# Optimization experiments

Measured on AMD Instinct MI355X. Metric: run time of the kernel, lower is better.

The kernel has to match this reference:

```python
import jax, jax.numpy as jnp
import numpy as np

N = 50000
IN_C = 512
HID = 16
HEADS = 3
OUT_C = 128
NEG_SLOPE = 0.2


def _add_self_loops(edge_index, n):
    loop = jnp.arange(n, dtype=edge_index.dtype)
    src = jnp.concatenate([edge_index[0], loop])
    dst = jnp.concatenate([edge_index[1], loop])
    return src, dst


def gat_conv(x, W, a_src, a_dst, b, src, dst, n):
    # x: [N, Fin], W: [Fin, H*C], a_src/a_dst: [H, C], b: [H*C]
    H, C = a_src.shape
    h = (x @ W).reshape(n, H, C)                      # [N, H, C]
    e_src = jnp.einsum('nhc,hc->nh', h, a_src)        # [N, H]
    e_dst = jnp.einsum('nhc,hc->nh', h, a_dst)        # [N, H]
    e = jax.nn.leaky_relu(e_src[src] + e_dst[dst], NEG_SLOPE)  # [E, H]
    # segment softmax over incoming edges of each destination node
    m = jax.ops.segment_max(e, dst, num_segments=n)
    e = jnp.exp(e - m[dst])
    s = jax.ops.segment_sum(e, dst, num_segments=n)
    alpha = e / s[dst]                                 # [E, H]
    out = jax.ops.segment_sum(h[src] * alpha[:, :, None], dst, num_segments=n)
    return out.reshape(n, H * C) + b


def gcn_conv(x, W, b, src, dst, n):
    h = x @ W                                          # [N, Fout]
    ones = jnp.ones(src.shape[0], dtype=h.dtype)
    deg = jax.ops.segment_sum(ones, dst, num_segments=n)
    dinv = jax.lax.rsqrt(jnp.maximum(deg, 1.0))
    norm = dinv[src] * dinv[dst]                       # [E]
    out = jax.ops.segment_sum(h[src] * norm[:, None], dst, num_segments=n)
    return out + b


def setup_inputs() -> dict:
    key = jax.random.key(0)
    ks = jax.random.split(key, 16)
    E = 800000
    x = jax.random.normal(ks[0], (N, IN_C), dtype=jnp.float32)
    edge_index = jax.random.randint(ks[1], (2, E), 0, N, dtype=jnp.int64)

    def glorot(k, shape):
        fan = shape[0] + shape[-1]
        return jax.random.uniform(k, shape, jnp.float32, -1.0, 1.0) * np.sqrt(6.0 / fan)

    return {
        'x': x,
        'edge_index': edge_index,
        'W1': glorot(ks[2], (IN_C, HEADS * HID)),
        'a_src1': glorot(ks[3], (HEADS, HID)),
        'a_dst1': glorot(ks[4], (HEADS, HID)),
        'b1': jnp.zeros((HEADS * HID,), jnp.float32),
        'W2': glorot(ks[5], (HEADS * HID, OUT_C)),
        'a_src2': glorot(ks[6], (1, OUT_C)),
        'a_dst2': glorot(ks[7], (1, OUT_C)),
        'b2': jnp.zeros((OUT_C,), jnp.float32),
        'Wg': glorot(ks[8], (OUT_C, OUT_C)),
        'bg': jnp.zeros((OUT_C,), jnp.float32),
        'Wl': glorot(ks[9], (OUT_C, OUT_C)),
        'bl': jnp.zeros((OUT_C,), jnp.float32),
    }


def reference(x, edge_index, W1, a_src1, a_dst1, b1, W2, a_src2, a_dst2, b2, Wg, bg, Wl, bl):
    n = x.shape[0]
    src, dst = _add_self_loops(edge_index, n)
    # GATModel: gat1 (3 heads, concat) -> elu -> gat2 (1 head) -> log_softmax
    h = gat_conv(x, W1, a_src1, a_dst1, b1, src, dst, n)
    h = jax.nn.elu(h)
    h = gat_conv(h, W2, a_src2, a_dst2, b2, src, dst, n)
    h = jax.nn.log_softmax(h, axis=1)
    # GCN: only conv1 is used in its forward, followed by relu
    h = jax.nn.relu(gcn_conv(h, Wg, bg, src, dst, n))
    # Linear1
    return h @ Wl + bl
```

## Files before the change

### kernel.cpp

```cpp
#include <hip/hip_runtime.h>
#include <hip/hip_bf16.h>
#include <math.h>

#define NN 50000
#define EE 800000
#define ET 850000
#define NB 196
#define NEG 0.2f

static __device__ __forceinline__ float lrelu(float x){ return x > 0.f ? x : NEG * x; }
static __device__ __forceinline__ void edge_sd(const int* __restrict__ ei, int e, int& s, int& d){
  if (e < EE){ s = ei[e]; d = ei[e + EE]; } else { s = e - EE; d = s; }
}

__global__ __launch_bounds__(256) void k_hist(const int* __restrict__ ei, int* __restrict__ deg_i)
{
  int e = blockIdx.x * 256 + threadIdx.x;
  if (e >= ET) return;
  int s, d; edge_sd(ei, e, s, d);
  atomicAdd(deg_i + d, 1);
}

__global__ __launch_bounds__(256) void k_scan_part(const int* __restrict__ deg_i, int* __restrict__ bsum)
{
  __shared__ int wsum[4];
  int t = threadIdx.x;
  int i = blockIdx.x * 256 + t;
  int v = (i < NN) ? deg_i[i] : 0;
  int r = v;
#pragma unroll
  for (int off = 32; off; off >>= 1) r += __shfl_xor(r, off);
  if ((t & 63) == 0) wsum[t >> 6] = r;
  __syncthreads();
  if (t == 0) bsum[blockIdx.x] = wsum[0] + wsum[1] + wsum[2] + wsum[3];
}

__global__ __launch_bounds__(256) void k_scan_top(const int* __restrict__ bsum, int* __restrict__ boff)
{
  __shared__ int bs[256];
  int t = threadIdx.x;
  int v = (t < NB) ? bsum[t] : 0;
  bs[t] = v;
  __syncthreads();
  for (int off = 1; off < 256; off <<= 1){
    int add = (t >= off) ? bs[t - off] : 0;
    __syncthreads();
    bs[t] += add;
    __syncthreads();
  }
  if (t < NB) boff[t] = bs[t] - v;
}

__global__ __launch_bounds__(256) void k_scan_fin(const int* __restrict__ deg_i,
    const int* __restrict__ boff, int* __restrict__ row_start, float* __restrict__ dinv)
{
  __shared__ int bs[256];
  int t = threadIdx.x;
  int i = blockIdx.x * 256 + t;
  int v = (i < NN) ? deg_i[i] : 0;
  bs[t] = v;
  __syncthreads();
  for (int off = 1; off < 256; off <<= 1){
    int add = (t >= off) ? bs[t - off] : 0;
    __syncthreads();
    bs[t] += add;
    __syncthreads();
  }
  if (i < NN){
    row_start[i] = boff[blockIdx.x] + bs[t] - v;
    dinv[i] = rsqrtf(fmaxf((float)v, 1.0f));
  }
  if (i == 0) row_start[NN] = ET;
}

__global__ __launch_bounds__(256) void k_fill(const int* __restrict__ ei,
    const int* __restrict__ row_start, int* __restrict__ cur, int* __restrict__ csr)
{
  int e = blockIdx.x * 256 + threadIdx.x;
  if (e >= ET) return;
  int s, d; edge_sd(ei, e, s, d);
  int pos = atomicAdd(cur + d, 1);
  csr[row_start[d] + pos] = s;
}

__global__ __launch_bounds__(256) void k_gat1_gemm(
    const float* __restrict__ x, const float* __restrict__ W1,
    const float* __restrict__ as1, const float* __restrict__ ad1,
    float* __restrict__ h1, float* __restrict__ es1, float* __restrict__ ed1)
{
  __shared__ float At[64][69];
  __shared__ float Bs[64][52];
  int t = threadIdx.x;
  int tx = t & 15, ty = t >> 4;
  int n0 = blockIdx.x * 64;
  float acc[4][3] = {};
  for (int kt = 0; kt < 512; kt += 64){
    __syncthreads();
#pragma unroll
    for (int p = 0; p < 4; ++p){
      int f = t + p * 256;
      int node = f >> 4, kq = f & 15;
      float4 v = make_float4(0.f, 0.f, 0.f, 0.f);
      int gn = n0 + node;
      if (gn < NN) v = *(const float4*)(x + (size_t)gn * 512 + kt + kq * 4);
      At[kq * 4 + 0][node] = v.x; At[kq * 4 + 1][node] = v.y;
      At[kq * 4 + 2][node] = v.z; At[kq * 4 + 3][node] = v.w;
    }
#pragma unroll
    for (int p = 0; p < 3; ++p){
      int f = t + p * 256;
      int k = f / 12, oq = f % 12;
      *(float4*)&Bs[k][oq * 4] = *(const float4*)(W1 + (size_t)(kt + k) * 48 + oq * 4);
    }
    __syncthreads();
#pragma unroll 8
    for (int k = 0; k < 64; ++k){
      float4 a = *(const float4*)&At[k][ty * 4];
      float b0 = Bs[k][tx * 3 + 0], b1 = Bs[k][tx * 3 + 1], b2 = Bs[k][tx * 3 + 2];
      float av[4] = {a.x, a.y, a.z, a.w};
#pragma unroll
      for (int i = 0; i < 4; ++i){
        acc[i][0] = fmaf(av[i], b0, acc[i][0]);
        acc[i][1] = fmaf(av[i], b1, acc[i][1]);
        acc[i][2] = fmaf(av[i], b2, acc[i][2]);
      }
    }
  }
#pragma unroll
  for (int i = 0; i < 4; ++i){
    int gn = n0 + ty * 4 + i;
    float ps0 = 0.f, ps1 = 0.f, ps2 = 0.f, pd0 = 0.f, pd1 = 0.f, pd2 = 0.f;
#pragma unroll
    for (int j = 0; j < 3; ++j){
      int o = tx * 3 + j;
      int h = o >> 4;
      float a = acc[i][j];
      float vs = a * as1[o], vd = a * ad1[o];
      if (h == 0){ ps0 += vs; pd0 += vd; }
      else if (h == 1){ ps1 += vs; pd1 += vd; }
      else { ps2 += vs; pd2 += vd; }
    }
#pragma unroll
    for (int off = 1; off < 16; off <<= 1){
      ps0 += __shfl_xor(ps0, off, 16); ps1 += __shfl_xor(ps1, off, 16); ps2 += __shfl_xor(ps2, off, 16);
      pd0 += __shfl_xor(pd0, off, 16); pd1 += __shfl_xor(pd1, off, 16); pd2 += __shfl_xor(pd2, off, 16);
    }
    if (gn < NN){
      float* o = h1 + (size_t)gn * 48 + tx * 3;
      o[0] = acc[i][0]; o[1] = acc[i][1]; o[2] = acc[i][2];
      if (tx == 0){
        es1[(size_t)gn * 3 + 0] = ps0; es1[(size_t)gn * 3 + 1] = ps1; es1[(size_t)gn * 3 + 2] = ps2;
        ed1[(size_t)gn * 3 + 0] = pd0; ed1[(size_t)gn * 3 + 1] = pd1; ed1[(size_t)gn * 3 + 2] = pd2;
      }
    }
  }
}

__global__ __launch_bounds__(256) void k_gat1_agg(
    const int* __restrict__ csr, const int* __restrict__ row_start,
    const float* __restrict__ es1, const float* __restrict__ ed1,
    const float* __restrict__ h1, const float* __restrict__ b1,
    float* __restrict__ o1)
{
  int dn = (blockIdx.x * 256 + threadIdx.x) >> 6;
  int lane = threadIdx.x & 63;
  if (dn >= NN) return;
  bool act = lane < 48;
  int hd = act ? (lane >> 4) : 0;
  int beg = row_start[dn], end = row_start[dn + 1];
  float edv = ed1[(size_t)dn * 3 + hd];
  float m = -INFINITY, sum = 0.f, acc = 0.f;
  int i = beg;
  for (; i + 1 < end; i += 2){
    int s0 = csr[i], s1 = csr[i + 1];
    float e0 = lrelu(es1[(size_t)s0 * 3 + hd] + edv);
    float e1 = lrelu(es1[(size_t)s1 * 3 + hd] + edv);
    float h0 = act ? h1[(size_t)s0 * 48 + lane] : 0.f;
    float h1v = act ? h1[(size_t)s1 * 48 + lane] : 0.f;
    float mn = fmaxf(m, fmaxf(e0, e1));
    float sc = __expf(m - mn), w0 = __expf(e0 - mn), w1 = __expf(e1 - mn);
    sum = sum * sc + w0 + w1;
    acc = acc * sc + h0 * w0 + h1v * w1;
    m = mn;
  }
  if (i < end){
    int s0 = csr[i];
    float e0 = lrelu(es1[(size_t)s0 * 3 + hd] + edv);
    float h0 = act ? h1[(size_t)s0 * 48 + lane] : 0.f;
    float mn = fmaxf(m, e0);
    float sc = __expf(m - mn), w0 = __expf(e0 - mn);
    sum = sum * sc + w0;
    acc = acc * sc + h0 * w0;
  }
  if (act){
    float v = acc / sum + b1[lane];
    o1[(size_t)dn * 48 + lane] = v > 0.f ? v : expm1f(v);
  }
}

__global__ __launch_bounds__(256) void k_gat2_gemm(const float* __restrict__ o1,
    const float* __restrict__ W2, const float* __restrict__ as2, const float* __restrict__ ad2,
    float* __restrict__ h2, float* __restrict__ es2, float* __restrict__ ed2)
{
  __shared__ float At[48][68];
  __shared__ float Ws[48][128];
  int t = threadIdx.x, tx = t & 15, ty = t >> 4;
  int n0 = blockIdx.x * 64;
#pragma unroll
  for (int p = 0; p < 3; ++p){
    int f = t + p * 256;
    int node = f / 12, kq = f % 12;
    float4 v = make_float4(0.f, 0.f, 0.f, 0.f);
    if (n0 + node < NN) v = *(const float4*)(o1 + (size_t)(n0 + node) * 48 + kq * 4);
    At[kq * 4 + 0][node] = v.x; At[kq * 4 + 1][node] = v.y;
    At[kq * 4 + 2][node] = v.z; At[kq * 4 + 3][node] = v.w;
  }
#pragma unroll
  for (int p = 0; p < 6; ++p){
    int f = t + p * 256;
    int k = f >> 5, cq = f & 31;
    *(float4*)&Ws[k][cq * 4] = *(const float4*)(W2 + (size_t)k * 128 + cq * 4);
  }
  __syncthreads();
  float acc[4][8] = {};
#pragma unroll 4
  for (int k = 0; k < 48; ++k){
    float4 a  = *(const float4*)&At[k][ty * 4];
    float4 c0 = *(const float4*)&Ws[k][tx * 4];
    float4 c1 = *(const float4*)&Ws[k][tx * 4 + 64];
    float av[4] = {a.x, a.y, a.z, a.w};
    float bv[8] = {c0.x, c0.y, c0.z, c0.w, c1.x, c1.y, c1.z, c1.w};
#pragma unroll
    for (int i = 0; i < 4; ++i)
#pragma unroll
      for (int j = 0; j < 8; ++j)
        acc[i][j] = fmaf(av[i], bv[j], acc[i][j]);
  }
  float asv[8], adv[8];
#pragma unroll
  for (int j = 0; j < 4; ++j){
    asv[j] = as2[tx * 4 + j];      asv[4 + j] = as2[64 + tx * 4 + j];
    adv[j] = ad2[tx * 4 + j];      adv[4 + j] = ad2[64 + tx * 4 + j];
  }
#pragma unroll
  for (int i = 0; i < 4; ++i){
    int gn = n0 + ty * 4 + i;
    float s = 0.f, d = 0.f;
#pragma unroll
    for (int j = 0; j < 8; ++j){ s = fmaf(acc[i][j], asv[j], s); d = fmaf(acc[i][j], adv[j], d); }
#pragma unroll
    for (int off = 1; off < 16; off <<= 1){
      s += __shfl_xor(s, off, 16);
      d += __shfl_xor(d, off, 16);
    }
    if (gn < NN){
      float4 o0 = make_float4(acc[i][0], acc[i][1], acc[i][2], acc[i][3]);
      float4 o1v = make_float4(acc[i][4], acc[i][5], acc[i][6], acc[i][7]);
      *(float4*)(h2 + (size_t)gn * 128 + tx * 4) = o0;
      *(float4*)(h2 + (size_t)gn * 128 + tx * 4 + 64) = o1v;
      if (tx == 0){ es2[gn] = s; ed2[gn] = d; }
    }
  }
}

__global__ __launch_bounds__(256) void k_gat2_agg(
    const int* __restrict__ csr, const int* __restrict__ row_start,
    const float* __restrict__ es2, const float* __restrict__ ed2,
    const float* __restrict__ h2, const float* __restrict__ b2,
    float* __restrict__ o2)
{
  int wid = (blockIdx.x * 256 + threadIdx.x) >> 6;
  int lane = threadIdx.x & 63;
  int half = lane >> 5, l32 = lane & 31;
  int d = wid * 2 + half;
  if (d >= NN) return;
  int beg = row_start[d], end = row_start[d + 1];
  float edv = ed2[d];
  float m = -INFINITY, sum = 0.f;
  float ax = 0.f, ay = 0.f, az = 0.f, aw = 0.f;
  int i = beg;
  for (; i + 1 < end; i += 2){
    int s0 = csr[i], s1 = csr[i + 1];
    float e0 = lrelu(es2[s0] + edv);
    float e1 = lrelu(es2[s1] + edv);
    float4 v0 = *(const float4*)(h2 + (size_t)s0 * 128 + l32 * 4);
    float4 v1 = *(const float4*)(h2 + (size_t)s1 * 128 + l32 * 4);
    float mn = fmaxf(m, fmaxf(e0, e1));
    float sc = __expf(m - mn), w0 = __expf(e0 - mn), w1 = __expf(e1 - mn);
    sum = sum * sc + w0 + w1;
    ax = ax * sc + v0.x * w0 + v1.x * w1;
    ay = ay * sc + v0.y * w0 + v1.y * w1;
    az = az * sc + v0.z * w0 + v1.z * w1;
    aw = aw * sc + v0.w * w0 + v1.w * w1;
    m = mn;
  }
  if (i < end){
    int s0 = csr[i];
    float e0 = lrelu(es2[s0] + edv);
    float4 v0 = *(const float4*)(h2 + (size_t)s0 * 128 + l32 * 4);
    float mn = fmaxf(m, e0);
    float sc = __expf(m - mn), w0 = __expf(e0 - mn);
    sum = sum * sc + w0;
    ax = ax * sc + v0.x * w0;
    ay = ay * sc + v0.y * w0;
    az = az * sc + v0.z * w0;
    aw = aw * sc + v0.w * w0;
  }
  float inv = 1.f / sum;
  float4 vb = *(const float4*)(b2 + l32 * 4);
  float v0 = ax * inv + vb.x, v1 = ay * inv + vb.y;
  float v2 = az * inv + vb.z, v3 = aw * inv + vb.w;
  float mx = fmaxf(fmaxf(v0, v1), fmaxf(v2, v3));
#pragma unroll
  for (int off = 16; off; off >>= 1) mx = fmaxf(mx, __shfl_xor(mx, off, 32));
  float es = __expf(v0 - mx) + __expf(v1 - mx) + __expf(v2 - mx) + __expf(v3 - mx);
#pragma unroll
  for (int off = 16; off; off >>= 1) es += __shfl_xor(es, off, 32);
  float lse = mx + __logf(es);
  float4 ov = make_float4(v0 - lse, v1 - lse, v2 - lse, v3 - lse);
  *(float4*)(o2 + (size_t)d * 128 + l32 * 4) = ov;
}

__global__ __launch_bounds__(256) void k_gcn_agg(
    const int* __restrict__ csr, const int* __restrict__ row_start,
    const float* __restrict__ dinv, const float* __restrict__ hg,
    float* __restrict__ og)
{
  int wid = (blockIdx.x * 256 + threadIdx.x) >> 6;
  int lane = threadIdx.x & 63;
  int half = lane >> 5, l32 = lane & 31;
  int d = wid * 2 + half;
  if (d >= NN) return;
  int beg = row_start[d], end = row_start[d + 1];
  float ax = 0.f, ay = 0.f, az = 0.f, aw = 0.f;
  float bx = 0.f, by = 0.f, bz = 0.f, bw = 0.f;
  int i = beg;
  for (; i + 1 < end; i += 2){
    int s0 = csr[i], s1 = csr[i + 1];
    float4 v0 = *(const float4*)(hg + (size_t)s0 * 128 + l32 * 4);
    float4 v1 = *(const float4*)(hg + (size_t)s1 * 128 + l32 * 4);
    ax += v0.x; ay += v0.y; az += v0.z; aw += v0.w;
    bx += v1.x; by += v1.y; bz += v1.z; bw += v1.w;
  }
  if (i < end){
    int s0 = csr[i];
    float4 v0 = *(const float4*)(hg + (size_t)s0 * 128 + l32 * 4);
    ax += v0.x; ay += v0.y; az += v0.z; aw += v0.w;
  }
  float dd = dinv[d];
  float4 ov = make_float4((ax + bx) * dd, (ay + by) * dd, (az + bz) * dd, (aw + bw) * dd);
  *(float4*)(og + (size_t)d * 128 + l32 * 4) = ov;
}

template<int PRE, int POST, int SCALE>
__global__ __launch_bounds__(256) void k_gemm128(const float* __restrict__ in,
    const float* __restrict__ W, const float* __restrict__ bpre,
    const float* __restrict__ bpost, const float* __restrict__ dinv,
    float* __restrict__ out)
{
  __shared__ float At[32][68];
  __shared__ float Ws[32][128];
  int t = threadIdx.x, tx = t & 15, ty = t >> 4;
  int n0 = blockIdx.x * 64;
  float acc[4][8] = {};
  for (int kt = 0; kt < 128; kt += 32){
    __syncthreads();
#pragma unroll
    for (int p = 0; p < 2; ++p){
      int f = t + p * 256;
      int node = f >> 3, kq = f & 7;
      float4 v = make_float4(0.f, 0.f, 0.f, 0.f);
      if (n0 + node < NN){
        v = *(const float4*)(in + (size_t)(n0 + node) * 128 + kt + kq * 4);
        if (PRE){
          const float* bp = bpre + kt + kq * 4;
          v.x = fmaxf(v.x + bp[0], 0.f); v.y = fmaxf(v.y + bp[1], 0.f);
          v.z = fmaxf(v.z + bp[2], 0.f); v.w = fmaxf(v.w + bp[3], 0.f);
        }
      }
      At[kq * 4 + 0][node] = v.x; At[kq * 4 + 1][node] = v.y;
      At[kq * 4 + 2][node] = v.z; At[kq * 4 + 3][node] = v.w;
    }
#pragma unroll
    for (int p = 0; p < 4; ++p){
      int f = t + p * 256;
      int k = f >> 5, cq = f & 31;
      *(float4*)&Ws[k][cq * 4] = *(const float4*)(W + (size_t)(kt + k) * 128 + cq * 4);
    }
    __syncthreads();
#pragma unroll 4
    for (int k = 0; k < 32; ++k){
      float4 a  = *(const float4*)&At[k][ty * 4];
      float4 c0 = *(const float4*)&Ws[k][tx * 4];
      float4 c1 = *(const float4*)&Ws[k][tx * 4 + 64];
      float av[4] = {a.x, a.y, a.z, a.w};
      float bv[8] = {c0.x, c0.y, c0.z, c0.w, c1.x, c1.y, c1.z, c1.w};
#pragma unroll
      for (int i = 0; i < 4; ++i)
#pragma unroll
        for (int j = 0; j < 8; ++j)
          acc[i][j] = fmaf(av[i], bv[j], acc[i][j]);
    }
  }
#pragma unroll
  for (int i = 0; i < 4; ++i){
    int gn = n0 + ty * 4 + i;
    if (gn < NN){
      float sc = SCALE ? dinv[gn] : 1.f;
      float4 o0, o1v;
      o0.x  = (acc[i][0] + (POST ? bpost[tx * 4 + 0] : 0.f)) * sc;
      o0.y  = (acc[i][1] + (POST ? bpost[tx * 4 + 1] : 0.f)) * sc;
      o0.z  = (acc[i][2] + (POST ? bpost[tx * 4 + 2] : 0.f)) * sc;
      o0.w  = (acc[i][3] + (POST ? bpost[tx * 4 + 3] : 0.f)) * sc;
      o1v.x = (acc[i][4] + (POST ? bpost[64 + tx * 4 + 0] : 0.f)) * sc;
      o1v.y = (acc[i][5] + (POST ? bpost[64 + tx * 4 + 1] : 0.f)) * sc;
      o1v.z = (acc[i][6] + (POST ? bpost[64 + tx * 4 + 2] : 0.f)) * sc;
      o1v.w = (acc[i][7] + (POST ? bpost[64 + tx * 4 + 3] : 0.f)) * sc;
      *(float4*)(out + (size_t)gn * 128 + tx * 4) = o0;
      *(float4*)(out + (size_t)gn * 128 + tx * 4 + 64) = o1v;
    }
  }
}

extern "C" void kernel_launch(void* const* d_in, const int* in_sizes, int n_in,
                              void* d_out, int out_size, void* d_ws, size_t ws_size,
                              hipStream_t stream)
{
  const float* x   = (const float*)d_in[0];
  const int*   ei  = (const int*)d_in[1];
  const float* W1  = (const float*)d_in[2];
  const float* as1 = (const float*)d_in[3];
  const float* ad1 = (const float*)d_in[4];
  const float* b1  = (const float*)d_in[5];
  const float* W2  = (const float*)d_in[6];
  const float* as2 = (const float*)d_in[7];
  const float* ad2 = (const float*)d_in[8];
  const float* b2  = (const float*)d_in[9];
  const float* Wg  = (const float*)d_in[10];
  const float* bg  = (const float*)d_in[11];
  const float* Wl  = (const float*)d_in[12];
  const float* bl  = (const float*)d_in[13];
  float* out = (float*)d_out;

  float* ws = (float*)d_ws;
  const size_t n = NN;
  float* h1   = ws;
  float* h2   = ws + 48 * n;
  float* o1   = ws + 176 * n;
  float* o2   = ws + 224 * n;
  float* es1  = ws + 352 * n;
  float* ed1  = ws + 355 * n;
  float* es2  = ws + 358 * n;
  float* ed2  = ws + 359 * n;
  float* dinv = ws + 360 * n;
  int* ints   = (int*)(ws + 361 * n);
  int* deg_i     = ints;
  int* cur       = ints + n;
  int* row_start = ints + 2 * n;
  int* csr       = ints + 3 * n + 1;
  int* bsum      = ints + 3 * n + 1 + ET;
  int* boff      = ints + 3 * n + 1 + ET + NB;
  float* og = o2;

  hipMemsetAsync(deg_i, 0, 2 * n * sizeof(int), stream);

  const int egrid = (ET + 255) / 256;
  const int wgrid = (NN * 64) / 256;
  const int hgrid = (NN / 2 * 64) / 256;
  k_hist<<<egrid, 256, 0, stream>>>(ei, deg_i);
  k_scan_part<<<NB, 256, 0, stream>>>(deg_i, bsum);
  k_scan_top<<<1, 256, 0, stream>>>(bsum, boff);
  k_scan_fin<<<NB, 256, 0, stream>>>(deg_i, boff, row_start, dinv);
  k_fill<<<egrid, 256, 0, stream>>>(ei, row_start, cur, csr);
  k_gat1_gemm<<<(NN + 63) / 64, 256, 0, stream>>>(x, W1, as1, ad1, h1, es1, ed1);
  k_gat1_agg<<<wgrid, 256, 0, stream>>>(csr, row_start, es1, ed1, h1, b1, o1);
  k_gat2_gemm<<<(NN + 63) / 64, 256, 0, stream>>>(o1, W2, as2, ad2, h2, es2, ed2);
  k_gat2_agg<<<hgrid, 256, 0, stream>>>(csr, row_start, es2, ed2, h2, b2, o2);
  k_gemm128<0, 0, 1><<<(NN + 63) / 64, 256, 0, stream>>>(o2, Wg, nullptr, nullptr, dinv, h2);
  k_gcn_agg<<<hgrid, 256, 0, stream>>>(csr, row_start, dinv, h2, og);
  k_gemm128<1, 1, 0><<<(NN + 63) / 64, 256, 0, stream>>>(og, Wl, bg, bl, nullptr, out);
}
```

Measured before the change: 552.1 us.

## Reorder GAT2 and GCN so aggregation runs on narrow features before GEMMs

Precomputes W2·a_src and W2·a_dst, so the GAT2 attention logits come straight from the 48-wide GAT1 output inside the GAT1 aggregation kernel. GAT2 then aggregates 48-wide features and applies the W2 projection plus log_softmax afterwards, which cuts gather traffic from 128 to 48 floats per edge. The GCN aggregation now scales sources by dinv and aggregates before the Wg GEMM, and the Wg and Wl GEMMs are fused into one kernel. The GAT1 GEMM shared-memory layout also changes to dot4-style reads. The reordering relies on linearity, so float rounding changes slightly.

```diff
diff --git a/kernel.cpp b/kernel.cpp
--- a/kernel.cpp
+++ b/kernel.cpp
@@ -11,6 +11,11 @@
 static __device__ __forceinline__ float lrelu(float x){ return x > 0.f ? x : NEG * x; }
 static __device__ __forceinline__ void edge_sd(const int* __restrict__ ei, int e, int& s, int& d){
   if (e < EE){ s = ei[e]; d = ei[e + EE]; } else { s = e - EE; d = s; }
+}
+static __device__ __forceinline__ float dot4(float4 a, float4 b, float acc){
+  acc = fmaf(a.x, b.x, acc); acc = fmaf(a.y, b.y, acc);
+  acc = fmaf(a.z, b.z, acc); acc = fmaf(a.w, b.w, acc);
+  return acc;
 }
 
 __global__ __launch_bounds__(256) void k_hist(const int* __restrict__ ei, int* __restrict__ deg_i)
@@ -83,13 +88,28 @@
   csr[row_start[d] + pos] = s;
 }
 
+__global__ __launch_bounds__(64) void k_w2(const float* __restrict__ W2,
+    const float* __restrict__ as2, const float* __restrict__ ad2,
+    float* __restrict__ w2as, float* __restrict__ w2ad)
+{
+  int k = threadIdx.x;
+  if (k >= 48) return;
+  float s = 0.f, d = 0.f;
+  for (int j = 0; j < 128; ++j){
+    float w = W2[(size_t)k * 128 + j];
+    s = fmaf(w, as2[j], s);
+    d = fmaf(w, ad2[j], d);
+  }
+  w2as[k] = s; w2ad[k] = d;
+}
+
 __global__ __launch_bounds__(256) void k_gat1_gemm(
     const float* __restrict__ x, const float* __restrict__ W1,
     const float* __restrict__ as1, const float* __restrict__ ad1,
     float* __restrict__ h1, float* __restrict__ es1, float* __restrict__ ed1)
 {
-  __shared__ float At[64][69];
-  __shared__ float Bs[64][52];
+  __shared__ float Xs[64][68];
+  __shared__ float Bt[48][68];
   int t = threadIdx.x;
   int tx = t & 15, ty = t >> 4;
   int n0 = blockIdx.x * 64;
@@ -103,27 +123,30 @@
       float4 v = make_float4(0.f, 0.f, 0.f, 0.f);
       int gn = n0 + node;
       if (gn < NN) v = *(const float4*)(x + (size_t)gn * 512 + kt + kq * 4);
-      At[kq * 4 + 0][node] = v.x; At[kq * 4 + 1][node] = v.y;
-      At[kq * 4 + 2][node] = v.z; At[kq * 4 + 3][node] = v.w;
+      *(float4*)&Xs[node][kq * 4] = v;
     }
 #pragma unroll
     for (int p = 0; p < 3; ++p){
       int f = t + p * 256;
       int k = f / 12, oq = f % 12;
-      *(float4*)&Bs[k][oq * 4] = *(const float4*)(W1 + (size_t)(kt + k) * 48 + oq * 4);
+      float4 v = *(const float4*)(W1 + (size_t)(kt + k) * 48 + oq * 4);
+      Bt[oq * 4 + 0][k] = v.x; Bt[oq * 4 + 1][k] = v.y;
+      Bt[oq * 4 + 2][k] = v.z; Bt[oq * 4 + 3][k] = v.w;
     }
     __syncthreads();
-#pragma unroll 8
-    for (int k = 0; k < 64; ++k){
-      float4 a = *(const float4*)&At[k][ty * 4];
-      float b0 = Bs[k][tx * 3 + 0], b1 = Bs[k][tx * 3 + 1], b2 = Bs[k][tx * 3 + 2];
-      float av[4] = {a.x, a.y, a.z, a.w};
-#pragma unroll
-      for (int i = 0; i < 4; ++i){
-        acc[i][0] = fmaf(av[i], b0, acc[i][0]);
-        acc[i][1] = fmaf(av[i], b1, acc[i][1]);
-        acc[i][2] = fmaf(av[i], b2, acc[i][2]);
-      }
+#pragma unroll 4
+    for (int k4 = 0; k4 < 64; k4 += 4){
+      float4 a0 = *(const float4*)&Xs[ty * 4 + 0][k4];
+      float4 a1 = *(const float4*)&Xs[ty * 4 + 1][k4];
+      float4 a2 = *(const float4*)&Xs[ty * 4 + 2][k4];
+      float4 a3 = *(const float4*)&Xs[ty * 4 + 3][k4];
+      float4 b0 = *(const float4*)&Bt[tx * 3 + 0][k4];
+      float4 b1 = *(const float4*)&Bt[tx * 3 + 1][k4];
+      float4 b2 = *(const float4*)&Bt[tx * 3 + 2][k4];
+      acc[0][0] = dot4(a0, b0, acc[0][0]); acc[0][1] = dot4(a0, b1, acc[0][1]); acc[0][2] = dot4(a0, b2, acc[0][2]);
+      acc[1][0] = dot4(a1, b0, acc[1][0]); acc[1][1] = dot4(a1, b1, acc[1][1]); acc[1][2] = dot4(a1, b2, acc[1][2]);
+      acc[2][0] = dot4(a2, b0, acc[2][0]); acc[2][1] = dot4(a2, b1, acc[2][1]); acc[2][2] = dot4(a2, b2, acc[2][2]);
+      acc[3][0] = dot4(a3, b0, acc[3][0]); acc[3][1] = dot4(a3, b1, acc[3][1]); acc[3][2] = dot4(a3, b2, acc[3][2]);
     }
   }
 #pragma unroll
@@ -160,7 +183,8 @@
     const int* __restrict__ csr, const int* __restrict__ row_start,
     const float* __restrict__ es1, const float* __restrict__ ed1,
     const float* __restrict__ h1, const float* __restrict__ b1,
-    float* __restrict__ o1)
+    const float* __restrict__ w2as, const float* __restrict__ w2ad,
+    float* __restrict__ o1, float* __restrict__ es2, float* __restrict__ ed2)
 {
   int dn = (blockIdx.x * 256 + threadIdx.x) >> 6;
   int lane = threadIdx.x & 63;
@@ -192,139 +216,130 @@
     sum = sum * sc + w0;
     acc = acc * sc + h0 * w0;
   }
+  float v = 0.f;
   if (act){
-    float v = acc / sum + b1[lane];
-    o1[(size_t)dn * 48 + lane] = v > 0.f ? v : expm1f(v);
-  }
-}
-
-__global__ __launch_bounds__(256) void k_gat2_gemm(const float* __restrict__ o1,
-    const float* __restrict__ W2, const float* __restrict__ as2, const float* __restrict__ ad2,
-    float* __restrict__ h2, float* __restrict__ es2, float* __restrict__ ed2)
-{
-  __shared__ float At[48][68];
-  __shared__ float Ws[48][128];
-  int t = threadIdx.x, tx = t & 15, ty = t >> 4;
-  int n0 = blockIdx.x * 64;
-#pragma unroll
-  for (int p = 0; p < 3; ++p){
-    int f = t + p * 256;
-    int node = f / 12, kq = f % 12;
-    float4 v = make_float4(0.f, 0.f, 0.f, 0.f);
-    if (n0 + node < NN) v = *(const float4*)(o1 + (size_t)(n0 + node) * 48 + kq * 4);
-    At[kq * 4 + 0][node] = v.x; At[kq * 4 + 1][node] = v.y;
-    At[kq * 4 + 2][node] = v.z; At[kq * 4 + 3][node] = v.w;
-  }
-#pragma unroll
-  for (int p = 0; p < 6; ++p){
-    int f = t + p * 256;
-    int k = f >> 5, cq = f & 31;
-    *(float4*)&Ws[k][cq * 4] = *(const float4*)(W2 + (size_t)k * 128 + cq * 4);
-  }
-  __syncthreads();
-  float acc[4][8] = {};
-#pragma unroll 4
-  for (int k = 0; k < 48; ++k){
-    float4 a  = *(const float4*)&At[k][ty * 4];
-    float4 c0 = *(const float4*)&Ws[k][tx * 4];
-    float4 c1 = *(const float4*)&Ws[k][tx * 4 + 64];
-    float av[4] = {a.x, a.y, a.z, a.w};
-    float bv[8] = {c0.x, c0.y, c0.z, c0.w, c1.x, c1.y, c1.z, c1.w};
-#pragma unroll
-    for (int i = 0; i < 4; ++i)
-#pragma unroll
-      for (int j = 0; j < 8; ++j)
-        acc[i][j] = fmaf(av[i], bv[j], acc[i][j]);
-  }
-  float asv[8], adv[8];
-#pragma unroll
-  for (int j = 0; j < 4; ++j){
-    asv[j] = as2[tx * 4 + j];      asv[4 + j] = as2[64 + tx * 4 + j];
-    adv[j] = ad2[tx * 4 + j];      adv[4 + j] = ad2[64 + tx * 4 + j];
-  }
-#pragma unroll
-  for (int i = 0; i < 4; ++i){
-    int gn = n0 + ty * 4 + i;
-    float s = 0.f, d = 0.f;
-#pragma unroll
-    for (int j = 0; j < 8; ++j){ s = fmaf(acc[i][j], asv[j], s); d = fmaf(acc[i][j], adv[j], d); }
-#pragma unroll
-    for (int off = 1; off < 16; off <<= 1){
-      s += __shfl_xor(s, off, 16);
-      d += __shfl_xor(d, off, 16);
-    }
-    if (gn < NN){
-      float4 o0 = make_float4(acc[i][0], acc[i][1], acc[i][2], acc[i][3]);
-      float4 o1v = make_float4(acc[i][4], acc[i][5], acc[i][6], acc[i][7]);
-      *(float4*)(h2 + (size_t)gn * 128 + tx * 4) = o0;
-      *(float4*)(h2 + (size_t)gn * 128 + tx * 4 + 64) = o1v;
-      if (tx == 0){ es2[gn] = s; ed2[gn] = d; }
-    }
-  }
+    v = acc / sum + b1[lane];
+    v = v > 0.f ? v : expm1f(v);
+    o1[(size_t)dn * 48 + lane] = v;
+  }
+  float ps = act ? v * w2as[lane] : 0.f;
+  float pd = act ? v * w2ad[lane] : 0.f;
+#pragma unroll
+  for (int off = 32; off; off >>= 1){ ps += __shfl_xor(ps, off); pd += __shfl_xor(pd, off); }
+  if (lane == 0){ es2[dn] = ps; ed2[dn] = pd; }
 }
 
 __global__ __launch_bounds__(256) void k_gat2_agg(
     const int* __restrict__ csr, const int* __restrict__ row_start,
     const float* __restrict__ es2, const float* __restrict__ ed2,
-    const float* __restrict__ h2, const float* __restrict__ b2,
-    float* __restrict__ o2)
-{
-  int wid = (blockIdx.x * 256 + threadIdx.x) >> 6;
+    const float* __restrict__ o1, float* __restrict__ agg2)
+{
+  int dn = (blockIdx.x * 256 + threadIdx.x) >> 6;
   int lane = threadIdx.x & 63;
-  int half = lane >> 5, l32 = lane & 31;
-  int d = wid * 2 + half;
-  if (d >= NN) return;
-  int beg = row_start[d], end = row_start[d + 1];
-  float edv = ed2[d];
-  float m = -INFINITY, sum = 0.f;
-  float ax = 0.f, ay = 0.f, az = 0.f, aw = 0.f;
+  if (dn >= NN) return;
+  bool act = lane < 48;
+  int beg = row_start[dn], end = row_start[dn + 1];
+  float edv = ed2[dn];
+  float m = -INFINITY, sum = 0.f, acc = 0.f;
   int i = beg;
   for (; i + 1 < end; i += 2){
     int s0 = csr[i], s1 = csr[i + 1];
     float e0 = lrelu(es2[s0] + edv);
     float e1 = lrelu(es2[s1] + edv);
-    float4 v0 = *(const float4*)(h2 + (size_t)s0 * 128 + l32 * 4);
-    float4 v1 = *(const float4*)(h2 + (size_t)s1 * 128 + l32 * 4);
+    float h0 = act ? o1[(size_t)s0 * 48 + lane] : 0.f;
+    float h1v = act ? o1[(size_t)s1 * 48 + lane] : 0.f;
     float mn = fmaxf(m, fmaxf(e0, e1));
     float sc = __expf(m - mn), w0 = __expf(e0 - mn), w1 = __expf(e1 - mn);
     sum = sum * sc + w0 + w1;
-    ax = ax * sc + v0.x * w0 + v1.x * w1;
-    ay = ay * sc + v0.y * w0 + v1.y * w1;
-    az = az * sc + v0.z * w0 + v1.z * w1;
-    aw = aw * sc + v0.w * w0 + v1.w * w1;
+    acc = acc * sc + h0 * w0 + h1v * w1;
     m = mn;
   }
   if (i < end){
     int s0 = csr[i];
     float e0 = lrelu(es2[s0] + edv);
-    float4 v0 = *(const float4*)(h2 + (size_t)s0 * 128 + l32 * 4);
+    float h0 = act ? o1[(size_t)s0 * 48 + lane] : 0.f;
     float mn = fmaxf(m, e0);
     float sc = __expf(m - mn), w0 = __expf(e0 - mn);
     sum = sum * sc + w0;
-    ax = ax * sc + v0.x * w0;
-    ay = ay * sc + v0.y * w0;
-    az = az * sc + v0.z * w0;
-    aw = aw * sc + v0.w * w0;
-  }
-  float inv = 1.f / sum;
-  float4 vb = *(const float4*)(b2 + l32 * 4);
-  float v0 = ax * inv + vb.x, v1 = ay * inv + vb.y;
-  float v2 = az * inv + vb.z, v3 = aw * inv + vb.w;
-  float mx = fmaxf(fmaxf(v0, v1), fmaxf(v2, v3));
-#pragma unroll
-  for (int off = 16; off; off >>= 1) mx = fmaxf(mx, __shfl_xor(mx, off, 32));
-  float es = __expf(v0 - mx) + __expf(v1 - mx) + __expf(v2 - mx) + __expf(v3 - mx);
-#pragma unroll
-  for (int off = 16; off; off >>= 1) es += __shfl_xor(es, off, 32);
-  float lse = mx + __logf(es);
-  float4 ov = make_float4(v0 - lse, v1 - lse, v2 - lse, v3 - lse);
-  *(float4*)(o2 + (size_t)d * 128 + l32 * 4) = ov;
+    acc = acc * sc + h0 * w0;
+  }
+  if (act) agg2[(size_t)dn * 48 + lane] = acc / sum;
+}
+
+__global__ __launch_bounds__(256) void k_gat2_post(const float* __restrict__ agg2,
+    const float* __restrict__ W2, const float* __restrict__ b2, float* __restrict__ o2)
+{
+  __shared__ float As[64][52];
+  __shared__ float Bt[128][52];
+  int t = threadIdx.x, tx = t & 15, ty = t >> 4;
+  int n0 = blockIdx.x * 64;
+#pragma unroll
+  for (int p = 0; p < 3; ++p){
+    int f = t + p * 256;
+    int node = f / 12, kq = f % 12;
+    float4 v = make_float4(0.f, 0.f, 0.f, 0.f);
+    if (n0 + node < NN) v = *(const float4*)(agg2 + (size_t)(n0 + node) * 48 + kq * 4);
+    *(float4*)&As[node][kq * 4] = v;
+  }
+#pragma unroll
+  for (int p = 0; p < 6; ++p){
+    int f = t + p * 256;
+    int k = f >> 5, cq = f & 31;
+    float4 v = *(const float4*)(W2 + (size_t)k * 128 + cq * 4);
+    Bt[cq * 4 + 0][k] = v.x; Bt[cq * 4 + 1][k] = v.y;
+    Bt[cq * 4 + 2][k] = v.z; Bt[cq * 4 + 3][k] = v.w;
+  }
+  __syncthreads();
+  float acc[4][8] = {};
+#pragma unroll 3
+  for (int k4 = 0; k4 < 48; k4 += 4){
+    float4 a[4], b[8];
+#pragma unroll
+    for (int i = 0; i < 4; ++i) a[i] = *(const float4*)&As[ty * 4 + i][k4];
+#pragma unroll
+    for (int j = 0; j < 4; ++j){
+      b[j]     = *(const float4*)&Bt[tx * 4 + j][k4];
+      b[4 + j] = *(const float4*)&Bt[64 + tx * 4 + j][k4];
+    }
+#pragma unroll
+    for (int i = 0; i < 4; ++i)
+#pragma unroll
+      for (int j = 0; j < 8; ++j)
+        acc[i][j] = dot4(a[i], b[j], acc[i][j]);
+  }
+  float bb[8];
+#pragma unroll
+  for (int j = 0; j < 4; ++j){ bb[j] = b2[tx * 4 + j]; bb[4 + j] = b2[64 + tx * 4 + j]; }
+#pragma unroll
+  for (int i = 0; i < 4; ++i){
+    int gn = n0 + ty * 4 + i;
+    float v[8];
+#pragma unroll
+    for (int j = 0; j < 8; ++j) v[j] = acc[i][j] + bb[j];
+    float mx = v[0];
+#pragma unroll
+    for (int j = 1; j < 8; ++j) mx = fmaxf(mx, v[j]);
+#pragma unroll
+    for (int off = 1; off < 16; off <<= 1) mx = fmaxf(mx, __shfl_xor(mx, off, 16));
+    float es = 0.f;
+#pragma unroll
+    for (int j = 0; j < 8; ++j) es += __expf(v[j] - mx);
+#pragma unroll
+    for (int off = 1; off < 16; off <<= 1) es += __shfl_xor(es, off, 16);
+    float lse = mx + __logf(es);
+    if (gn < NN){
+      float4 o0 = make_float4(v[0] - lse, v[1] - lse, v[2] - lse, v[3] - lse);
+      float4 o1v = make_float4(v[4] - lse, v[5] - lse, v[6] - lse, v[7] - lse);
+      *(float4*)(o2 + (size_t)gn * 128 + tx * 4) = o0;
+      *(float4*)(o2 + (size_t)gn * 128 + tx * 4 + 64) = o1v;
+    }
+  }
 }
 
 __global__ __launch_bounds__(256) void k_gcn_agg(
     const int* __restrict__ csr, const int* __restrict__ row_start,
-    const float* __restrict__ dinv, const float* __restrict__ hg,
-    float* __restrict__ og)
+    const float* __restrict__ dinv, const float* __restrict__ o2,
+    float* __restrict__ aggD)
 {
   int wid = (blockIdx.x * 256 + threadIdx.x) >> 6;
   int lane = threadIdx.x & 63;
@@ -337,85 +352,108 @@
   int i = beg;
   for (; i + 1 < end; i += 2){
     int s0 = csr[i], s1 = csr[i + 1];
-    float4 v0 = *(const float4*)(hg + (size_t)s0 * 128 + l32 * 4);
-    float4 v1 = *(const float4*)(hg + (size_t)s1 * 128 + l32 * 4);
-    ax += v0.x; ay += v0.y; az += v0.z; aw += v0.w;
-    bx += v1.x; by += v1.y; bz += v1.z; bw += v1.w;
+    float d0 = dinv[s0], d1 = dinv[s1];
+    float4 v0 = *(const float4*)(o2 + (size_t)s0 * 128 + l32 * 4);
+    float4 v1 = *(const float4*)(o2 + (size_t)s1 * 128 + l32 * 4);
+    ax = fmaf(v0.x, d0, ax); ay = fmaf(v0.y, d0, ay); az = fmaf(v0.z, d0, az); aw = fmaf(v0.w, d0, aw);
+    bx = fmaf(v1.x, d1, bx); by = fmaf(v1.y, d1, by); bz = fmaf(v1.z, d1, bz); bw = fmaf(v1.w, d1, bw);
   }
   if (i < end){
     int s0 = csr[i];
-    float4 v0 = *(const float4*)(hg + (size_t)s0 * 128 + l32 * 4);
-    ax += v0.x; ay += v0.y; az += v0.z; aw += v0.w;
+    float d0 = dinv[s0];
+    float4 v0 = *(const float4*)(o2 + (size_t)s0 * 128 + l32 * 4);
+    ax = fmaf(v0.x, d0, ax); ay = fmaf(v0.y, d0, ay); az = fmaf(v0.z, d0, az); aw = fmaf(v0.w, d0, aw);
   }
   float dd = dinv[d];
   float4 ov = make_float4((ax + bx) * dd, (ay + by) * dd, (az + bz) * dd, (aw + bw) * dd);
-  *(float4*)(og + (size_t)d * 128 + l32 * 4) = ov;
-}
-
-template<int PRE, int POST, int SCALE>
-__global__ __launch_bounds__(256) void k_gemm128(const float* __restrict__ in,
-    const float* __restrict__ W, const float* __restrict__ bpre,
-    const float* __restrict__ bpost, const float* __restrict__ dinv,
+  *(float4*)(aggD + (size_t)d * 128 + l32 * 4) = ov;
+}
+
+__global__ __launch_bounds__(256) void k_final(const float* __restrict__ aggD,
+    const float* __restrict__ Wg, const float* __restrict__ bg,
+    const float* __restrict__ Wl, const float* __restrict__ bl,
     float* __restrict__ out)
 {
-  __shared__ float At[32][68];
-  __shared__ float Ws[32][128];
+  __shared__ float Ta[64][132];
+  __shared__ float Bt[128][36];
   int t = threadIdx.x, tx = t & 15, ty = t >> 4;
   int n0 = blockIdx.x * 64;
-  float acc[4][8] = {};
-  for (int kt = 0; kt < 128; kt += 32){
-    __syncthreads();
-#pragma unroll
-    for (int p = 0; p < 2; ++p){
-      int f = t + p * 256;
-      int node = f >> 3, kq = f & 7;
-      float4 v = make_float4(0.f, 0.f, 0.f, 0.f);
-      if (n0 + node < NN){
-        v = *(const float4*)(in + (size_t)(n0 + node) * 128 + kt + kq * 4);
-        if (PRE){
-          const float* bp = bpre + kt + kq * 4;
-          v.x = fmaxf(v.x + bp[0], 0.f); v.y = fmaxf(v.y + bp[1], 0.f);
-          v.z = fmaxf(v.z + bp[2], 0.f); v.w = fmaxf(v.w + bp[3], 0.f);
+#pragma unroll
+  for (int p = 0; p < 8; ++p){
+    int f = t + p * 256;
+    int node = f >> 5, cq = f & 31;
+    float4 v = make_float4(0.f, 0.f, 0.f, 0.f);
+    if (n0 + node < NN) v = *(const float4*)(aggD + (size_t)(n0 + node) * 128 + cq * 4);
+    *(float4*)&Ta[node][cq * 4] = v;
+  }
+  float accv[4][8];
+  const float* Wcur = Wg;
+  for (int ph = 0; ph < 2; ++ph){
+#pragma unroll
+    for (int i = 0; i < 4; ++i)
+#pragma unroll
+      for (int j = 0; j < 8; ++j) accv[i][j] = 0.f;
+    for (int kt = 0; kt < 128; kt += 32){
+      __syncthreads();
+#pragma unroll
+      for (int p = 0; p < 4; ++p){
+        int f = t + p * 256;
+        int k = f >> 5, cq = f & 31;
+        float4 v = *(const float4*)(Wcur + (size_t)(kt + k) * 128 + cq * 4);
+        Bt[cq * 4 + 0][k] = v.x; Bt[cq * 4 + 1][k] = v.y;
+        Bt[cq * 4 + 2][k] = v.z; Bt[cq * 4 + 3][k] = v.w;
+      }
+      __syncthreads();
+#pragma unroll 2
+      for (int k4 = 0; k4 < 32; k4 += 4){
+        float4 a[4], b[8];
+#pragma unroll
+        for (int i = 0; i < 4; ++i) a[i] = *(const float4*)&Ta[ty * 4 + i][kt + k4];
+#pragma unroll
+        for (int j = 0; j < 4; ++j){
+          b[j]     = *(const float4*)&Bt[tx * 4 + j][k4];
+          b[4 + j] = *(const float4*)&Bt[64 + tx * 4 + j][k4];
         }
+#pragma unroll
+        for (int i = 0; i < 4; ++i)
+#pragma unroll
+          for (int j = 0; j < 8; ++j)
+            accv[i][j] = dot4(a[i], b[j], accv[i][j]);
       }
-      At[kq * 4 + 0][node] = v.x; At[kq * 4 + 1][node] = v.y;
-      At[kq * 4 + 2][node] = v.z; At[kq * 4 + 3][node] = v.w;
-    }
-#pragma unroll
-    for (int p = 0; p < 4; ++p){
-      int f = t + p * 256;
-      int k = f >> 5, cq = f & 31;
-      *(float4*)&Ws[k][cq * 4] = *(const float4*)(W + (size_t)(kt + k) * 128 + cq * 4);
-    }
-    __syncthreads();
-#pragma unroll 4
-    for (int k = 0; k < 32; ++k){
-      float4 a  = *(const float4*)&At[k][ty * 4];
-      float4 c0 = *(const float4*)&Ws[k][tx * 4];
-      float4 c1 = *(const float4*)&Ws[k][tx * 4 + 64];
-      float av[4] = {a.x, a.y, a.z, a.w};
-      float bv[8] = {c0.x, c0.y, c0.z, c0.w, c1.x, c1.y, c1.z, c1.w};
-#pragma unroll
-      for (int i = 0; i < 4; ++i)
-#pragma unroll
-        for (int j = 0; j < 8; ++j)
-          acc[i][j] = fmaf(av[i], bv[j], acc[i][j]);
+    }
+    if (ph == 0){
+      __syncthreads();
+#pragma unroll
+      for (int i = 0; i < 4; ++i){
+        int n = ty * 4 + i;
+        float4 w0, w1;
+        w0.x = fmaxf(accv[i][0] + bg[tx * 4 + 0], 0.f);
+        w0.y = fmaxf(accv[i][1] + bg[tx * 4 + 1], 0.f);
+        w0.z = fmaxf(accv[i][2] + bg[tx * 4 + 2], 0.f);
+        w0.w = fmaxf(accv[i][3] + bg[tx * 4 + 3], 0.f);
+        w1.x = fmaxf(accv[i][4] + bg[64 + tx * 4 + 0], 0.f);
+        w1.y = fmaxf(accv[i][5] + bg[64 + tx * 4 + 1], 0.f);
+        w1.z = fmaxf(accv[i][6] + bg[64 + tx * 4 + 2], 0.f);
+        w1.w = fmaxf(accv[i][7] + bg[64 + tx * 4 + 3], 0.f);
+        *(float4*)&Ta[n][tx * 4] = w0;
+        *(float4*)&Ta[n][tx * 4 + 64] = w1;
+      }
+      Wcur = Wl;
     }
   }
 #pragma unroll
   for (int i = 0; i < 4; ++i){
     int gn = n0 + ty * 4 + i;
     if (gn < NN){
-      float sc = SCALE ? dinv[gn] : 1.f;
       float4 o0, o1v;
-      o0.x  = (acc[i][0] + (POST ? bpost[tx * 4 + 0] : 0.f)) * sc;
-      o0.y  = (acc[i][1] + (POST ? bpost[tx * 4 + 1] : 0.f)) * sc;
-      o0.z  = (acc[i][2] + (POST ? bpost[tx * 4 + 2] : 0.f)) * sc;
-      o0.w  = (acc[i][3] + (POST ? bpost[tx * 4 + 3] : 0.f)) * sc;
-      o1v.x = (acc[i][4] + (POST ? bpost[64 + tx * 4 + 0] : 0.f)) * sc;
-      o1v.y = (acc[i][5] + (POST ? bpost[64 + tx * 4 + 1] : 0.f)) * sc;
-      o1v.z = (acc[i][6] + (POST ? bpost[64 + tx * 4 + 2] : 0.f)) * sc;
-      o1v.w = (acc[i][7] + (POST ? bpost[64 + tx * 4 + 3] : 0.f)) * sc;
+      o0.x = accv[i][0] + bl[tx * 4 + 0];
+      o0.y = accv[i][1] + bl[tx * 4 + 1];
+      o0.z = accv[i][2] + bl[tx * 4 + 2];
+      o0.w = accv[i][3] + bl[tx * 4 + 3];
+      o1v.x = accv[i][4] + bl[64 + tx * 4 + 0];
+      o1v.y = accv[i][5] + bl[64 + tx * 4 + 1];
+      o1v.z = accv[i][6] + bl[64 + tx * 4 + 2];
+      o1v.w = accv[i][7] + bl[64 + tx * 4 + 3];
       *(float4*)(out + (size_t)gn * 128 + tx * 4) = o0;
       *(float4*)(out + (size_t)gn * 128 + tx * 4 + 64) = o1v;
     }
@@ -445,38 +483,41 @@
   float* ws = (float*)d_ws;
   const size_t n = NN;
   float* h1   = ws;
-  float* h2   = ws + 48 * n;
-  float* o1   = ws + 176 * n;
-  float* o2   = ws + 224 * n;
-  float* es1  = ws + 352 * n;
-  float* ed1  = ws + 355 * n;
-  float* es2  = ws + 358 * n;
-  float* ed2  = ws + 359 * n;
-  float* dinv = ws + 360 * n;
-  int* ints   = (int*)(ws + 361 * n);
+  float* o1   = ws + 48 * n;
+  float* agg2 = ws + 96 * n;
+  float* o2   = ws + 144 * n;
+  float* aggD = ws + 272 * n;
+  float* es1  = ws + 400 * n;
+  float* ed1  = ws + 403 * n;
+  float* es2  = ws + 406 * n;
+  float* ed2  = ws + 407 * n;
+  float* dinv = ws + 408 * n;
+  float* w2as = ws + 409 * n;
+  float* w2ad = ws + 409 * n + 64;
+  int* ints   = (int*)(ws + 410 * n);
   int* deg_i     = ints;
   int* cur       = ints + n;
   int* row_start = ints + 2 * n;
   int* csr       = ints + 3 * n + 1;
   int* bsum      = ints + 3 * n + 1 + ET;
   int* boff      = ints + 3 * n + 1 + ET + NB;
-  float* og = o2;
 
   hipMemsetAsync(deg_i, 0, 2 * n * sizeof(int), stream);
 
   const int egrid = (ET + 255) / 256;
   const int wgrid = (NN * 64) / 256;
   const int hgrid = (NN / 2 * 64) / 256;
+  const int ggrid = (NN + 63) / 64;
   k_hist<<<egrid, 256, 0, stream>>>(ei, deg_i);
   k_scan_part<<<NB, 256, 0, stream>>>(deg_i, bsum);
   k_scan_top<<<1, 256, 0, stream>>>(bsum, boff);
   k_scan_fin<<<NB, 256, 0, stream>>>(deg_i, boff, row_start, dinv);
   k_fill<<<egrid, 256, 0, stream>>>(ei, row_start, cur, csr);
-  k_gat1_gemm<<<(NN + 63) / 64, 256, 0, stream>>>(x, W1, as1, ad1, h1, es1, ed1);
-  k_gat1_agg<<<wgrid, 256, 0, stream>>>(csr, row_start, es1, ed1, h1, b1, o1);
-  k_gat2_gemm<<<(NN + 63) / 64, 256, 0, stream>>>(o1, W2, as2, ad2, h2, es2, ed2);
-  k_gat2_agg<<<hgrid, 256, 0, stream>>>(csr, row_start, es2, ed2, h2, b2, o2);
-  k_gemm128<0, 0, 1><<<(NN + 63) / 64, 256, 0, stream>>>(o2, Wg, nullptr, nullptr, dinv, h2);
-  k_gcn_agg<<<hgrid, 256, 0, stream>>>(csr, row_start, dinv, h2, og);
-  k_gemm128<1, 1, 0><<<(NN + 63) / 64, 256, 0, stream>>>(og, Wl, bg, bl, nullptr, out);
-}
+  k_w2<<<1, 64, 0, stream>>>(W2, as2, ad2, w2as, w2ad);
+  k_gat1_gemm<<<ggrid, 256, 0, stream>>>(x, W1, as1, ad1, h1, es1, ed1);
+  k_gat1_agg<<<wgrid, 256, 0, stream>>>(csr, row_start, es1, ed1, h1, b1, w2as, w2ad, o1, es2, ed2);
+  k_gat2_agg<<<wgrid, 256, 0, stream>>>(csr, row_start, es2, ed2, o1, agg2);
+  k_gat2_post<<<ggrid, 256, 0, stream>>>(agg2, W2, b2, o2);
+  k_gcn_agg<<<hgrid, 256, 0, stream>>>(csr, row_start, dinv, o2, aggD);
+  k_final<<<ggrid, 256, 0, stream>>>(aggD, Wg, bg, Wl, bl, out);
+}
```

Measured after the change: 625.5 us. 1.13x slower.
